# Kernel tuning notes

Measured on AMD Instinct MI355X. Metric: run time of the kernel, lower is better.

The kernel has to match this reference:

```python
import jax, jax.numpy as jnp
import numpy as np

B, N, D, NH, L, DFF = 2, 2048, 256, 8, 4, 1024
DH = D // NH
FACTOR = 0.5 / float(np.sqrt(DH))  # == 1/sqrt(4*DH), matches q/k feature dim 4*d_head
EPS = 1e-5


def _ln(x, g, b):
    m = x.mean(-1, keepdims=True)
    v = ((x - m) ** 2).mean(-1, keepdims=True)
    return (x - m) * jax.lax.rsqrt(v + EPS) * g + b


def setup_inputs() -> dict:
    key = jax.random.key(0)
    ks = jax.random.split(key, 16)
    s = 0.05
    r = lambda i, shape: jax.random.normal(ks[i], shape, dtype=jnp.float32)
    return {
        "H": r(0, (B, N, D)),
        "V": r(1, (B, N, 3, D)),
        "D_batch": r(2, (B, N, N)),
        "rbf_feat": r(3, (L, B, 1, N, N)),
        "H_mask": jnp.ones((B, N), dtype=bool),
        "ln1_g": jnp.ones((L, D)), "ln1_b": jnp.zeros((L, D)),
        "ln2_g": jnp.ones((L, D)), "ln2_b": jnp.zeros((L, D)),
        "Wq": r(4, (L, D, 4 * D)) * s, "bq": jnp.zeros((L, 4 * D)),
        "Wk": r(5, (L, D, 4 * D)) * s, "bk": jnp.zeros((L, 4 * D)),
        "Wv": r(6, (L, D, D)) * s, "bv": jnp.zeros((L, D)),
        "Wvv": r(7, (L, D, D)) * s,
        "Wo": r(8, (L, D, D)) * s, "bo": jnp.zeros((L, D)),
        "Wvo": r(9, (L, D, D)) * s,
        "Wlv": r(10, (L, D, 2 * D)) * s,
        "W1": r(11, (L, 2 * D, DFF)) * s, "b1": jnp.zeros((L, DFF)),
        "W2": r(12, (L, DFF, 2 * D)) * s, "b2": jnp.zeros((L, 2 * D)),
    }


def _stack_forward(H, V, D_batch, rbf_feat, H_mask, ln1_g, ln1_b, ln2_g, ln2_b,
                   Wq, bq, Wk, bk, Wv, bv, Wvv, Wo, bo, Wvo, Wlv, W1, b1, W2, b2):
    b, n = H.shape[:2]
    mask = H_mask[:, None, None, :]       # [B,1,1,N] masks key columns
    base_bias = D_batch[:, None]          # [B,1,N,N]

    def step(carry, xs):
        H, V = carry
        (rbf, g1, be1, g2, be2, wq, bq_, wk, bk_, wv, bv_, wvv,
         wo, bo_, wvo, wlv, w1, b1_, w2, b2_) = xs
        # --- self-attention sublayer (pre-LN on scalar stream only) ---
        Hn = _ln(H, g1, be1)
        Hq = (Hn @ wq + bq_).reshape(b, n, NH, 4 * DH)
        Hk = (Hn @ wk + bk_).reshape(b, n, NH, 4 * DH)
        Hv = (Hn @ wv + bv_).reshape(b, n, NH, DH)
        Vv = (V @ wvv).reshape(b, n, 3, NH, DH)
        Vv = jnp.swapaxes(Vv, 2, 3).reshape(b, n, NH, 3 * DH)
        V_attn = jnp.concatenate([Hv, Vv], axis=-1)        # [B,N,H,4*DH]
        bias = jnp.where(mask, rbf + base_bias, -jnp.inf)  # [B,1,N,N]
        scores = jnp.einsum('bnhd,bmhd->bhnm', Hq, Hk) * FACTOR + bias
        attn = jax.nn.softmax(scores, axis=-1)
        res = jnp.einsum('bhnm,bmhd->bnhd', attn, V_attn)  # [B,N,H,4*DH]
        H_res = res[..., :DH].reshape(b, n, D)
        V_res = jnp.swapaxes(res[..., DH:].reshape(b, n, NH, 3, DH), 2, 3).reshape(b, n, 3, D)
        H = H + (H_res @ wo + bo_)
        V = V + V_res @ wvo
        # --- GVP FFN sublayer (pre-LN on scalar stream only) ---
        Hn = _ln(H, g2, be2)
        Vp = V @ wlv                                       # [B,N,3,2D]
        V1, V2 = Vp[..., :D], Vp[..., D:]
        scaler = jnp.concatenate([Hn, jnp.linalg.norm(V1, axis=-2)], axis=-1)
        sc = jax.nn.silu(scaler @ w1 + b1_) @ w2 + b2_
        H = H + sc[..., :D]
        V = V + sc[..., D:][..., None, :] * V2             # vector_act='none'
        return (H, V), None

    xs = (rbf_feat, ln1_g, ln1_b, ln2_g, ln2_b, Wq, bq, Wk, bk, Wv, bv, Wvv,
          Wo, bo, Wvo, Wlv, W1, b1, W2, b2)
    (H, V), _ = jax.lax.scan(step, (H, V), xs)
    return H, V


def reference(H, V, D_batch, rbf_feat, H_mask, ln1_g, ln1_b, ln2_g, ln2_b,
              Wq, bq, Wk, bk, Wv, bv, Wvv, Wo, bo, Wvo, Wlv, W1, b1, W2, b2):
    return _stack_forward(H, V, D_batch, rbf_feat, H_mask, ln1_g, ln1_b, ln2_g, ln2_b,
                          Wq, bq, Wk, bk, Wv, bv, Wvv, Wo, bo, Wvo, Wlv, W1, b1, W2, b2)
```

## Files before the change

kernel.cpp:

```cpp
#include <hip/hip_runtime.h>
#include <math.h>

static constexpr int B_  = 2;
static constexpr int N_  = 2048;
static constexpr int D_  = 256;
static constexpr int NH_ = 8;
static constexpr int L_  = 4;
static constexpr int DH_ = 32;
static constexpr int DQ_ = 128;
static constexpr float FACTOR_ = 0.08838834764831845f;
static constexpr float LOG2E_  = 1.4426950408889634f;
static constexpr float EPS_ = 1e-5f;

typedef short    short8   __attribute__((ext_vector_type(8)));
typedef unsigned short us4 __attribute__((ext_vector_type(4)));
typedef unsigned short us8 __attribute__((ext_vector_type(8)));
typedef float    f32x4    __attribute__((ext_vector_type(4)));
typedef unsigned short us;

__device__ __forceinline__ us f2b(float f) {
  unsigned u = __float_as_uint(f);
  unsigned r = u + 0x7FFF + ((u >> 16) & 1);
  return (us)(r >> 16);
}
__device__ __forceinline__ float b2f(us u) {
  return __uint_as_float(((unsigned)u) << 16);
}
__device__ __forceinline__ float e2(float x) {
  return __builtin_amdgcn_exp2f(x);
}
__device__ __forceinline__ void gl_lds16(const void* g, void* l) {
  __builtin_amdgcn_global_load_lds(
      (const __attribute__((address_space(1))) void*)g,
      (__attribute__((address_space(3))) void*)l, 16, 0, 0);
}

__global__ __launch_bounds__(256) void ln_kernel(const float* __restrict__ X,
    const float* __restrict__ g, const float* __restrict__ b,
    us* __restrict__ Y) {
  __shared__ float r1[256], r2[256];
  int row = blockIdx.x, tid = threadIdx.x;
  float x = X[(size_t)row * D_ + tid];
  r1[tid] = x; r2[tid] = x * x;
  __syncthreads();
  for (int s = 128; s > 0; s >>= 1) {
    if (tid < s) { r1[tid] += r1[tid + s]; r2[tid] += r2[tid + s]; }
    __syncthreads();
  }
  float mean = r1[0] * (1.0f / D_);
  float var  = r2[0] * (1.0f / D_) - mean * mean;
  float inv  = rsqrtf(var + EPS_);
  Y[(size_t)row * D_ + tid] = f2b((x - mean) * inv * g[tid] + b[tid]);
}

__global__ __launch_bounds__(256) void conv_bf16(const float* __restrict__ X,
    us* __restrict__ Y) {
  size_t i = ((size_t)blockIdx.x * 256 + threadIdx.x) * 4;
  float4 v = *(const float4*)&X[i];
  us4 o = { f2b(v.x), f2b(v.y), f2b(v.z), f2b(v.w) };
  *(us4*)&Y[i] = o;
}

__global__ __launch_bounds__(256) void biascomb(const float* __restrict__ R,
    const float* __restrict__ Dq, us* __restrict__ Out) {
  size_t i = ((size_t)blockIdx.x * 256 + threadIdx.x) * 8;
  float4 r0 = *(const float4*)&R[i];
  float4 r1 = *(const float4*)&R[i + 4];
  float4 d0 = *(const float4*)&Dq[i];
  float4 d1 = *(const float4*)&Dq[i + 4];
  us8 o = { f2b((r0.x + d0.x) * LOG2E_), f2b((r0.y + d0.y) * LOG2E_),
            f2b((r0.z + d0.z) * LOG2E_), f2b((r0.w + d0.w) * LOG2E_),
            f2b((r1.x + d1.x) * LOG2E_), f2b((r1.y + d1.y) * LOG2E_),
            f2b((r1.z + d1.z) * LOG2E_), f2b((r1.w + d1.w) * LOG2E_) };
  *(us8*)&Out[i] = o;
}

struct WConvDesc {
  const float* src[9];
  unsigned dst[9];
  int K[9];
  int N[9];
  int start[10];
};
__global__ __launch_bounds__(256) void wconv_kernel(WConvDesc d, us* __restrict__ Wb) {
  __shared__ float T[64][65];
  int bid = blockIdx.x, tid = threadIdx.x;
  int j = 0;
  #pragma unroll
  for (int q = 0; q < 8; q++) if (bid >= d.start[q + 1]) j = q + 1;
  int t = bid - d.start[j];
  int K = d.K[j], N = d.N[j];
  int tpr = N >> 6;
  int tk = t / tpr, tn = t - tk * tpr;
  const float* src = d.src[j];
  us* dst = Wb + d.dst[j];
  #pragma unroll
  for (int i = 0; i < 4; i++) {
    int r = i * 16 + (tid >> 4), c = (tid & 15) * 4;
    *(float4*)&T[r][c] = *(const float4*)&src[(size_t)(tk * 64 + r) * N + tn * 64 + c];
  }
  __syncthreads();
  #pragma unroll
  for (int i = 0; i < 4; i++) {
    int n = i * 16 + (tid >> 4), k = (tid & 15) * 4;
    us4 o = { f2b(T[k][n]), f2b(T[k + 1][n]), f2b(T[k + 2][n]), f2b(T[k + 3][n]) };
    *(us4*)&dst[(size_t)(tn * 64 + n) * K + tk * 64 + k] = o;
  }
}

template<int BIG, int BIAS, int ACC, int SILU, int WF, int WB, int QKV>
__global__ __launch_bounds__(256, 2) void gemm_v2(const us* __restrict__ A,
    const us* __restrict__ Wt, const float* __restrict__ bias,
    const float* __restrict__ bias2, const float* __restrict__ bias3,
    float* __restrict__ Cf, us* __restrict__ Cb,
    int M, int K, int Nc, float oscale) {
  constexpr int BM  = BIG ? 128 : 64;
  constexpr int NF  = BIG ? 4 : 2;
  constexpr int WS  = NF * 16;
  constexpr int NLD = BM / 32;
  __shared__ us As[2][BM * 64];
  __shared__ us Bs[2][BM * 64];
  const int tid = threadIdx.x;
  const int w = tid >> 6, l = tid & 63;
  const int lx = l & 15, ly = l >> 4;
  const int wr = w >> 1, wc = w & 1;
  const int bn = blockIdx.x, bm = blockIdx.y;
  const int swz = (lx & 7) << 4;
  const char* Ag = (const char*)A + (size_t)(bm * BM) * K * 2;
  const char* Bg = (const char*)Wt + (size_t)(bn * BM) * K * 2;
  const size_t rowb = (size_t)K * 2;

  #define GSTAGE(buf, k0)                                                     \
    do {                                                                      \
      _Pragma("unroll")                                                       \
      for (int j = 0; j < NLD; j++) {                                         \
        int o = j * 4096 + tid * 16;                                          \
        int r = o >> 7, cb = o & 127;                                         \
        int sc = cb ^ ((r & 7) << 4);                                         \
        gl_lds16(Ag + (size_t)r * rowb + (size_t)(k0) * 2 + sc,               \
                 &As[buf][(j * 4096 + w * 1024) >> 1]);                       \
        gl_lds16(Bg + (size_t)r * rowb + (size_t)(k0) * 2 + sc,               \
                 &Bs[buf][(j * 4096 + w * 1024) >> 1]);                       \
      }                                                                       \
    } while (0)

  f32x4 acc[NF][NF];
  #pragma unroll
  for (int i = 0; i < NF; i++)
    #pragma unroll
    for (int j = 0; j < NF; j++) acc[i][j] = (f32x4){0.f, 0.f, 0.f, 0.f};

  int cur = 0;
  GSTAGE(0, 0);
  __syncthreads();
  for (int k0 = 0; k0 < K; k0 += 64) {
    if (k0 + 64 < K) GSTAGE(cur ^ 1, k0 + 64);
    #pragma unroll
    for (int s = 0; s < 2; s++) {
      short8 af[NF], bf[NF];
      #pragma unroll
      for (int mt = 0; mt < NF; mt++)
        af[mt] = *(const short8*)
            &As[cur][(((wr * WS + mt * 16 + lx) * 128) + ((s * 64 + ly * 16) ^ swz)) >> 1];
      #pragma unroll
      for (int nt = 0; nt < NF; nt++)
        bf[nt] = *(const short8*)
            &Bs[cur][(((wc * WS + nt * 16 + lx) * 128) + ((s * 64 + ly * 16) ^ swz)) >> 1];
      __builtin_amdgcn_s_setprio(1);
      #pragma unroll
      for (int mt = 0; mt < NF; mt++)
        #pragma unroll
        for (int nt = 0; nt < NF; nt++)
          acc[mt][nt] = __builtin_amdgcn_mfma_f32_16x16x32_bf16(af[mt], bf[nt], acc[mt][nt], 0, 0, 0);
      __builtin_amdgcn_s_setprio(0);
    }
    __syncthreads();
    cur ^= 1;
  }
  #undef GSTAGE

  #pragma unroll
  for (int nt = 0; nt < NF; nt++) {
    const int n = bn * BM + wc * WS + nt * 16 + lx;
    float bval = 0.f, osc = oscale;
    if (QKV) {
      if (n < 1024)      { bval = bias[n]; }
      else if (n < 2048) { bval = bias2[n - 1024]; osc = 1.0f; }
      else               { bval = bias3[n - 2048]; osc = 1.0f; }
    } else if (BIAS) {
      bval = bias[n];
    }
    #pragma unroll
    for (int mt = 0; mt < NF; mt++) {
      #pragma unroll
      for (int r = 0; r < 4; r++) {
        const int m = bm * BM + wr * WS + mt * 16 + ly * 4 + r;
        float v = acc[mt][nt][r] + bval;
        if (SILU) v = v / (1.f + __expf(-v));
        size_t idx = (size_t)m * Nc + n;
        if (ACC) v += Cf[idx];
        if (WF) Cf[idx] = v;
        if (WB) Cb[idx] = f2b(v * osc);
      }
    }
  }
}

__global__ __launch_bounds__(256, 2) void gemm_wo(const us* __restrict__ Hres,
    const us* __restrict__ Vres, const us* __restrict__ WtO,
    const us* __restrict__ WtVO, const float* __restrict__ bo,
    float* __restrict__ Hs, float* __restrict__ Vs, us* __restrict__ Vb) {
  constexpr int K = 256, Nc = 256;
  __shared__ us As[2][64 * 64];
  __shared__ us Bs[2][64 * 64];
  const int tid = threadIdx.x;
  const int w = tid >> 6, l = tid & 63;
  const int lx = l & 15, ly = l >> 4;
  const int wr = w >> 1, wc = w & 1;
  const int bn = blockIdx.x, bm = blockIdx.y;
  const bool isH = bm < 64;
  const int mb = isH ? bm : bm - 64;
  const int swz = (lx & 7) << 4;
  const char* Ag = (const char*)(isH ? Hres : Vres) + (size_t)(mb * 64) * K * 2;
  const char* Bg = (const char*)(isH ? WtO : WtVO) + (size_t)(bn * 64) * K * 2;
  const size_t rowb = (size_t)K * 2;

  #define GSTAGE(buf, k0)                                                     \
    do {                                                                      \
      _Pragma("unroll")                                                       \
      for (int j = 0; j < 2; j++) {                                           \
        int o = j * 4096 + tid * 16;                                          \
        int r = o >> 7, cb = o & 127;                                         \
        int sc = cb ^ ((r & 7) << 4);                                         \
        gl_lds16(Ag + (size_t)r * rowb + (size_t)(k0) * 2 + sc,               \
                 &As[buf][(j * 4096 + w * 1024) >> 1]);                       \
        gl_lds16(Bg + (size_t)r * rowb + (size_t)(k0) * 2 + sc,               \
                 &Bs[buf][(j * 4096 + w * 1024) >> 1]);                       \
      }                                                                       \
    } while (0)

  f32x4 acc[2][2];
  #pragma unroll
  for (int i = 0; i < 2; i++)
    #pragma unroll
    for (int j = 0; j < 2; j++) acc[i][j] = (f32x4){0.f, 0.f, 0.f, 0.f};

  int cur = 0;
  GSTAGE(0, 0);
  __syncthreads();
  for (int k0 = 0; k0 < K; k0 += 64) {
    if (k0 + 64 < K) GSTAGE(cur ^ 1, k0 + 64);
    #pragma unroll
    for (int s = 0; s < 2; s++) {
      short8 af[2], bf[2];
      #pragma unroll
      for (int mt = 0; mt < 2; mt++)
        af[mt] = *(const short8*)
            &As[cur][(((wr * 32 + mt * 16 + lx) * 128) + ((s * 64 + ly * 16) ^ swz)) >> 1];
      #pragma unroll
      for (int nt = 0; nt < 2; nt++)
        bf[nt] = *(const short8*)
            &Bs[cur][(((wc * 32 + nt * 16 + lx) * 128) + ((s * 64 + ly * 16) ^ swz)) >> 1];
      __builtin_amdgcn_s_setprio(1);
      #pragma unroll
      for (int mt = 0; mt < 2; mt++)
        #pragma unroll
        for (int nt = 0; nt < 2; nt++)
          acc[mt][nt] = __builtin_amdgcn_mfma_f32_16x16x32_bf16(af[mt], bf[nt], acc[mt][nt], 0, 0, 0);
      __builtin_amdgcn_s_setprio(0);
    }
    __syncthreads();
    cur ^= 1;
  }
  #undef GSTAGE

  #pragma unroll
  for (int nt = 0; nt < 2; nt++) {
    const int n = bn * 64 + wc * 32 + nt * 16 + lx;
    const float bval = isH ? bo[n] : 0.f;
    #pragma unroll
    for (int mt = 0; mt < 2; mt++) {
      #pragma unroll
      for (int r = 0; r < 4; r++) {
        const int m = mb * 64 + wr * 32 + mt * 16 + ly * 4 + r;
        size_t idx = (size_t)m * Nc + n;
        float v = acc[mt][nt][r] + bval;
        if (isH) {
          Hs[idx] += v;
        } else {
          float nv = Vs[idx] + v;
          Vs[idx] = nv;
          Vb[idx] = f2b(nv);
        }
      }
    }
  }
}

__global__ __launch_bounds__(256, 2) void gemm_w2(const us* __restrict__ A,
    const us* __restrict__ Wt, const float* __restrict__ b2,
    const float* __restrict__ Vp, float* __restrict__ Hs,
    float* __restrict__ Vs, us* __restrict__ Vb) {
  constexpr int K = 1024, Nc = 512;
  __shared__ us As[2][64 * 64];
  __shared__ us Bs[2][64 * 64];
  const int tid = threadIdx.x;
  const int w = tid >> 6, l = tid & 63;
  const int lx = l & 15, ly = l >> 4;
  const int wr = w >> 1, wc = w & 1;
  const int bn = blockIdx.x, bm = blockIdx.y;
  const int swz = (lx & 7) << 4;
  const char* Ag = (const char*)A + (size_t)(bm * 64) * K * 2;
  const char* Bg = (const char*)Wt + (size_t)(bn * 64) * K * 2;
  const size_t rowb = (size_t)K * 2;

  #define GSTAGE(buf, k0)                                                     \
    do {                                                                      \
      _Pragma("unroll")                                                       \
      for (int j = 0; j < 2; j++) {                                           \
        int o = j * 4096 + tid * 16;                                          \
        int r = o >> 7, cb = o & 127;                                         \
        int sc = cb ^ ((r & 7) << 4);                                         \
        gl_lds16(Ag + (size_t)r * rowb + (size_t)(k0) * 2 + sc,               \
                 &As[buf][(j * 4096 + w * 1024) >> 1]);                       \
        gl_lds16(Bg + (size_t)r * rowb + (size_t)(k0) * 2 + sc,               \
                 &Bs[buf][(j * 4096 + w * 1024) >> 1]);                       \
      }                                                                      \
    } while (0)

  f32x4 acc[2][2];
  #pragma unroll
  for (int i = 0; i < 2; i++)
    #pragma unroll
    for (int j = 0; j < 2; j++) acc[i][j] = (f32x4){0.f, 0.f, 0.f, 0.f};

  int cur = 0;
  GSTAGE(0, 0);
  __syncthreads();
  for (int k0 = 0; k0 < K; k0 += 64) {
    if (k0 + 64 < K) GSTAGE(cur ^ 1, k0 + 64);
    #pragma unroll
    for (int s = 0; s < 2; s++) {
      short8 af[2], bf[2];
      #pragma unroll
      for (int mt = 0; mt < 2; mt++)
        af[mt] = *(const short8*)
            &As[cur][(((wr * 32 + mt * 16 + lx) * 128) + ((s * 64 + ly * 16) ^ swz)) >> 1];
      #pragma unroll
      for (int nt = 0; nt < 2; nt++)
        bf[nt] = *(const short8*)
            &Bs[cur][(((wc * 32 + nt * 16 + lx) * 128) + ((s * 64 + ly * 16) ^ swz)) >> 1];
      __builtin_amdgcn_s_setprio(1);
      #pragma unroll
      for (int mt = 0; mt < 2; mt++)
        #pragma unroll
        for (int nt = 0; nt < 2; nt++)
          acc[mt][nt] = __builtin_amdgcn_mfma_f32_16x16x32_bf16(af[mt], bf[nt], acc[mt][nt], 0, 0, 0);
      __builtin_amdgcn_s_setprio(0);
    }
    __syncthreads();
    cur ^= 1;
  }
  #undef GSTAGE

  const bool isH = (bn < 4);
  #pragma unroll
  for (int nt = 0; nt < 2; nt++) {
    const int n = bn * 64 + wc * 32 + nt * 16 + lx;
    const float bval = b2[n];
    #pragma unroll
    for (int mt = 0; mt < 2; mt++) {
      #pragma unroll
      for (int r = 0; r < 4; r++) {
        const int m = bm * 64 + wr * 32 + mt * 16 + ly * 4 + r;
        float v = acc[mt][nt][r] + bval;
        if (isH) {
          Hs[(size_t)m * D_ + n] += v;
        } else {
          const int j = n - 256;
          #pragma unroll
          for (int c = 0; c < 3; c++) {
            size_t vi = ((size_t)m * 3 + c) * D_ + j;
            float nv = Vs[vi] + v * Vp[((size_t)m * 3 + c) * 512 + 256 + j];
            Vs[vi] = nv;
            Vb[vi] = f2b(nv);
          }
        }
      }
    }
  }
}

__global__ __launch_bounds__(256) void pack_vattn_t(const us* __restrict__ QKVb,
    const us* __restrict__ Vv, us* __restrict__ Vt) {
  __shared__ us T[64][136];
  const int bid = blockIdx.x;
  const int nt = bid & 31, hh = (bid >> 5) & 7, b = bid >> 8;
  const int n0 = nt * 64;
  const int tid = threadIdx.x;
  {
    const int nn = tid >> 2, part = tid & 3;
    const size_t row = (size_t)(b * N_ + n0 + nn);
    const us* src = (part == 0) ? (QKVb + row * 2304 + 2048 + hh * DH_)
                                : (Vv + (row * 3 + (part - 1)) * D_ + hh * DH_);
    #pragma unroll
    for (int jj = 0; jj < 32; jj += 8)
      *(us8*)&T[nn][part * 32 + jj] = *(const us8*)(src + jj);
  }
  __syncthreads();
  const int d = tid >> 1, half = tid & 1;
  size_t ob = ((size_t)(b * NH_ + hh) * DQ_ + d) * (size_t)N_ + n0 + half * 32;
  #pragma unroll
  for (int i = 0; i < 32; i += 8) {
    us8 o;
    #pragma unroll
    for (int e = 0; e < 8; e++) o[e] = T[half * 32 + i + e][d];
    *(us8*)&Vt[ob + i] = o;
  }
}

__global__ __launch_bounds__(256, 2) void attn_mfma(
    const us* __restrict__ QKVb,
    const us* __restrict__ Vtb,
    const us* __restrict__ bias,
    us* __restrict__ Hres,
    us* __restrict__ Vres) {
  __shared__ us Kt[2][8192];
  __shared__ us Vt[2][8192];
  __shared__ us Plds[4][16][72];
  const int bid = blockIdx.x;
  const int h  = bid >> 6;
  const int g  = bid & 63;
  const int b  = g >> 5;
  const int qt = g & 31;
  const int tid = threadIdx.x;
  const int w  = tid >> 6;
  const int l  = tid & 63;
  const int lx = l & 15;
  const int ly = l >> 4;
  const int qrow = qt * 64 + w * 16 + lx;
  const int swz = (lx & 7) << 4;

  short8 qf[4];
  {
    const us* qp = QKVb + (size_t)(b * N_ + qrow) * 2304 + h * DQ_ + ly * 8;
    #pragma unroll
    for (int s = 0; s < 4; s++) qf[s] = *(const short8*)(qp + s * 32);
  }
  const char* kg = (const char*)QKVb + (size_t)b * N_ * 4608 + 2048 + h * 256;
  const char* vg = (const char*)(Vtb + ((size_t)(b * NH_ + h) * DQ_) * (size_t)N_);
  const us* bbase = bias + ((size_t)b * N_ + qrow) * N_;

  #define STAGE(buf, m0)                                                      \
    do {                                                                      \
      _Pragma("unroll")                                                       \
      for (int j = 0; j < 4; j++) {                                           \
        int o = j * 4096 + tid * 16;                                          \
        int r = o >> 8, cb = o & 255;                                         \
        int scb = cb ^ ((r & 7) << 4);                                        \
        gl_lds16(kg + (size_t)((m0) + r) * 4608 + scb,                        \
                 &Kt[buf][(j * 4096 + w * 1024) >> 1]);                       \
      }                                                                       \
      _Pragma("unroll")                                                       \
      for (int j = 0; j < 4; j++) {                                           \
        int o = j * 4096 + tid * 16;                                          \
        int r = o >> 7, cb = o & 127;                                         \
        int scb = cb ^ ((r & 7) << 4);                                        \
        gl_lds16(vg + (size_t)r * (N_ * 2) + (size_t)(m0) * 2 + scb,          \
                 &Vt[buf][(j * 4096 + w * 1024) >> 1]);                       \
      }                                                                       \
    } while (0)

  float m_run = -3.0e38f, l_run = 0.f;
  f32x4 oacc[8];
  #pragma unroll
  for (int i = 0; i < 8; i++) oacc[i] = (f32x4){0.f, 0.f, 0.f, 0.f};

  int cur = 0;
  STAGE(0, 0);
  us4 bb[4];
  #pragma unroll
  for (int t = 0; t < 4; t++) bb[t] = *(const us4*)(bbase + t * 16 + ly * 4);
  __syncthreads();

  for (int mc0 = 0; mc0 < N_; mc0 += 64) {
    us4 bbn[4];
    if (mc0 + 64 < N_) {
      STAGE(cur ^ 1, mc0 + 64);
      #pragma unroll
      for (int t = 0; t < 4; t++)
        bbn[t] = *(const us4*)(bbase + mc0 + 64 + t * 16 + ly * 4);
    }
    f32x4 sacc[4];
    #pragma unroll
    for (int t = 0; t < 4; t++) sacc[t] = (f32x4){0.f, 0.f, 0.f, 0.f};
    __builtin_amdgcn_s_setprio(1);
    #pragma unroll
    for (int t = 0; t < 4; t++) {
      #pragma unroll
      for (int s = 0; s < 4; s++) {
        const short8 kf = *(const short8*)
            &Kt[cur][((t * 16 + lx) * 256 + ((s * 64 + ly * 16) ^ swz)) >> 1];
        sacc[t] = __builtin_amdgcn_mfma_f32_16x16x32_bf16(kf, qf[s], sacc[t], 0, 0, 0);
      }
    }
    __builtin_amdgcn_s_setprio(0);
    float pvv[16];
    #pragma unroll
    for (int t = 0; t < 4; t++) {
      pvv[t*4+0] = sacc[t][0] + b2f(bb[t][0]);
      pvv[t*4+1] = sacc[t][1] + b2f(bb[t][1]);
      pvv[t*4+2] = sacc[t][2] + b2f(bb[t][2]);
      pvv[t*4+3] = sacc[t][3] + b2f(bb[t][3]);
    }
    float a8[8], a4[4];
    #pragma unroll
    for (int i = 0; i < 8; i++) a8[i] = fmaxf(pvv[i], pvv[i + 8]);
    #pragma unroll
    for (int i = 0; i < 4; i++) a4[i] = fmaxf(a8[i], a8[i + 4]);
    float mloc = fmaxf(fmaxf(a4[0], a4[1]), fmaxf(a4[2], a4[3]));
    if (!__all(mloc - m_run <= 11.54f)) {
      mloc = fmaxf(mloc, __shfl_xor(mloc, 16, 64));
      mloc = fmaxf(mloc, __shfl_xor(mloc, 32, 64));
      float m_new = fmaxf(m_run, mloc);
      float scale = e2(m_run - m_new);
      l_run *= scale;
      #pragma unroll
      for (int i = 0; i < 8; i++) {
        oacc[i][0] *= scale; oacc[i][1] *= scale;
        oacc[i][2] *= scale; oacc[i][3] *= scale;
      }
      m_run = m_new;
    }
    float s8[8], s4[4];
    #pragma unroll
    for (int i = 0; i < 16; i++) pvv[i] = e2(pvv[i] - m_run);
    #pragma unroll
    for (int i = 0; i < 8; i++) s8[i] = pvv[i] + pvv[i + 8];
    #pragma unroll
    for (int i = 0; i < 4; i++) s4[i] = s8[i] + s8[i + 4];
    l_run += (s4[0] + s4[1]) + (s4[2] + s4[3]);
    #pragma unroll
    for (int t = 0; t < 4; t++) {
      us4 pk = { f2b(pvv[t*4+0]), f2b(pvv[t*4+1]), f2b(pvv[t*4+2]), f2b(pvv[t*4+3]) };
      *(us4*)&Plds[w][lx][t * 16 + ly * 4] = pk;
    }
    short8 pf0 = *(const short8*)&Plds[w][lx][ly * 8];
    short8 pf1 = *(const short8*)&Plds[w][lx][32 + ly * 8];
    __builtin_amdgcn_s_setprio(1);
    #pragma unroll
    for (int dt = 0; dt < 8; dt++) {
      const int rb = (dt * 16 + lx) * 128;
      const short8 vf0 = *(const short8*)&Vt[cur][(rb + ((ly * 16) ^ swz)) >> 1];
      const short8 vf1 = *(const short8*)&Vt[cur][(rb + ((64 + ly * 16) ^ swz)) >> 1];
      oacc[dt] = __builtin_amdgcn_mfma_f32_16x16x32_bf16(vf0, pf0, oacc[dt], 0, 0, 0);
      oacc[dt] = __builtin_amdgcn_mfma_f32_16x16x32_bf16(vf1, pf1, oacc[dt], 0, 0, 0);
    }
    __builtin_amdgcn_s_setprio(0);
    __syncthreads();
    cur ^= 1;
    if (mc0 + 64 < N_) {
      #pragma unroll
      for (int t = 0; t < 4; t++) bb[t] = bbn[t];
    }
  }
  #undef STAGE
  l_run += __shfl_xor(l_run, 16, 64);
  l_run += __shfl_xor(l_run, 32, 64);
  float inv = 1.0f / l_run;
  const size_t row = (size_t)(b * N_ + qrow);
  #pragma unroll
  for (int dt = 0; dt < 8; dt++) {
    const int d0 = dt * 16 + ly * 4;
    us4 pk = { f2b(oacc[dt][0] * inv), f2b(oacc[dt][1] * inv),
               f2b(oacc[dt][2] * inv), f2b(oacc[dt][3] * inv) };
    if (d0 < 32) {
      *(us4*)&Hres[row * D_ + h * DH_ + d0] = pk;
    } else {
      const int c = (d0 - DH_) >> 5, dd = (d0 - DH_) & 31;
      *(us4*)&Vres[(row * 3 + c) * D_ + h * DH_ + dd] = pk;
    }
  }
}

__global__ __launch_bounds__(256) void ln2scaler(const float* __restrict__ H,
    const float* __restrict__ g, const float* __restrict__ b,
    const float* __restrict__ Vp, us* __restrict__ scal) {
  __shared__ float r1[256], r2[256];
  size_t row = blockIdx.x;
  int j = threadIdx.x;
  float x = H[row * D_ + j];
  r1[j] = x; r2[j] = x * x;
  __syncthreads();
  for (int s = 128; s > 0; s >>= 1) {
    if (j < s) { r1[j] += r1[j + s]; r2[j] += r2[j + s]; }
    __syncthreads();
  }
  float mean = r1[0] * (1.0f / D_);
  float var  = r2[0] * (1.0f / D_) - mean * mean;
  float inv  = rsqrtf(var + EPS_);
  scal[row * 512 + j] = f2b((x - mean) * inv * g[j] + b[j]);
  float a  = Vp[(row * 3 + 0) * 512 + j];
  float c1 = Vp[(row * 3 + 1) * 512 + j];
  float c2 = Vp[(row * 3 + 2) * 512 + j];
  scal[row * 512 + D_ + j] = f2b(sqrtf(a * a + c1 * c1 + c2 * c2));
}

extern "C" void kernel_launch(void* const* d_in, const int* in_sizes, int n_in,
                              void* d_out, int out_size, void* d_ws, size_t ws_size,
                              hipStream_t stream) {
  const float* H_in = (const float*)d_in[0];
  const float* V_in = (const float*)d_in[1];
  const float* Db   = (const float*)d_in[2];
  const float* rbf  = (const float*)d_in[3];
  const float* ln1g = (const float*)d_in[5];
  const float* ln1b = (const float*)d_in[6];
  const float* ln2g = (const float*)d_in[7];
  const float* ln2b = (const float*)d_in[8];
  const float* Wq  = (const float*)d_in[9];
  const float* bq  = (const float*)d_in[10];
  const float* Wk  = (const float*)d_in[11];
  const float* bk  = (const float*)d_in[12];
  const float* Wv  = (const float*)d_in[13];
  const float* bv  = (const float*)d_in[14];
  const float* Wvv = (const float*)d_in[15];
  const float* Wo  = (const float*)d_in[16];
  const float* bo  = (const float*)d_in[17];
  const float* Wvo = (const float*)d_in[18];
  const float* Wlv = (const float*)d_in[19];
  const float* W1  = (const float*)d_in[20];
  const float* b1  = (const float*)d_in[21];
  const float* W2  = (const float*)d_in[22];
  const float* b2  = (const float*)d_in[23];

  const size_t HN = (size_t)B_ * N_ * D_;
  const size_t VN = HN * 3;
  float* Hs = (float*)d_out;
  float* Vs = (float*)d_out + HN;
  float* ws = (float*)d_ws;
  us*    bias_b = (us*)ws;
  us*    Wb     = (us*)(ws + 4194304);
  us*    Vb     = (us*)(ws + 5177344);
  us*    Hnb    = (us*)(ws + 6750208);
  us*    QKVb   = (us*)(ws + 7274496);
  us*    Vtb    = (us*)(ws + 11993088);
  us*    Vvb    = (us*)(ws + 14090240);
  us*    Hres_b = (us*)(ws + 6750208);
  us*    Vres_b = (us*)(ws + 14090240);
  float* Vp     = ws + 7274496;
  us*    scal_b = (us*)(ws + 13565952);
  us*    midb   = (us*)(ws + 15014528);

  hipMemcpyAsync(Hs, H_in, HN * sizeof(float), hipMemcpyDeviceToDevice, stream);
  hipMemcpyAsync(Vs, V_in, VN * sizeof(float), hipMemcpyDeviceToDevice, stream);
  conv_bf16<<<3072, 256, 0, stream>>>(V_in, Vb);

  const int ROWS  = B_ * N_;
  static const int wKs[9] = {256,256,256,256,256,256,256,512,1024};
  static const int wNs[9] = {1024,1024,256,256,256,256,512,1024,512};
  static const unsigned wOff[9] = {0,262144,524288,589824,655360,720896,786432,917504,1441792};
  static const int wStart[10] = {0,64,128,144,160,176,192,224,352,480};

  for (int l = 0; l < L_; ++l) {
    WConvDesc dsc;
    const float* srcs[9] = {
      Wq  + (size_t)l * 256 * 1024, Wk  + (size_t)l * 256 * 1024,
      Wv  + (size_t)l * 256 * 256,  Wvv + (size_t)l * 256 * 256,
      Wo  + (size_t)l * 256 * 256,  Wvo + (size_t)l * 256 * 256,
      Wlv + (size_t)l * 256 * 512,  W1  + (size_t)l * 512 * 1024,
      W2  + (size_t)l * 1024 * 512 };
    for (int j = 0; j < 9; j++) {
      dsc.src[j] = srcs[j]; dsc.dst[j] = wOff[j];
      dsc.K[j] = wKs[j]; dsc.N[j] = wNs[j]; dsc.start[j] = wStart[j];
    }
    dsc.start[9] = wStart[9];
    wconv_kernel<<<480, 256, 0, stream>>>(dsc, Wb);
    biascomb<<<4096, 256, 0, stream>>>(rbf + (size_t)l * B_ * N_ * N_, Db, bias_b);
    if (l == 0)
      ln_kernel<<<ROWS, 256, 0, stream>>>(Hs, ln1g, ln1b, Hnb);

    gemm_v2<1,0,0,0,0,1,1><<<dim3(18, 32), 256, 0, stream>>>(
        Hnb, Wb + wOff[0], bq + l * 1024, bk + l * 1024, bv + l * 256,
        nullptr, QKVb, 4096, 256, 2304, FACTOR_ * LOG2E_);
    gemm_v2<0,0,0,0,0,1,0><<<dim3(4, 192), 256, 0, stream>>>(
        Vb, Wb + wOff[3], nullptr, nullptr, nullptr, nullptr, Vvb, 12288, 256, 256, 1.f);
    pack_vattn_t<<<512, 256, 0, stream>>>(QKVb, Vvb, Vtb);
    attn_mfma<<<512, 256, 0, stream>>>(QKVb, Vtb, bias_b, Hres_b, Vres_b);
    gemm_wo<<<dim3(4, 256), 256, 0, stream>>>(
        Hres_b, Vres_b, Wb + wOff[4], Wb + wOff[5], bo + l * 256, Hs, Vs, Vb);
    gemm_v2<0,0,0,0,1,0,0><<<dim3(8, 192), 256, 0, stream>>>(
        Vb, Wb + wOff[6], nullptr, nullptr, nullptr, Vp, nullptr, 12288, 256, 512, 1.f);
    ln2scaler<<<ROWS, 256, 0, stream>>>(Hs, ln2g + l * D_, ln2b + l * D_, Vp, scal_b);
    gemm_v2<0,1,0,1,0,1,0><<<dim3(16, 64), 256, 0, stream>>>(
        scal_b, Wb + wOff[7], b1 + l * 1024, nullptr, nullptr, nullptr, midb, 4096, 512, 1024, 1.f);
    gemm_w2<<<dim3(8, 64), 256, 0, stream>>>(
        midb, Wb + wOff[8], b2 + l * 512, Vp, Hs, Vs, Vb);
    if (l < 3)
      ln_kernel<<<ROWS, 256, 0, stream>>>(Hs, ln1g + (l + 1) * D_,
                                          ln1b + (l + 1) * D_, Hnb);
  }
}
```

Baseline: 808.6 us.

## Register-staged single-buffer K/V in attention and rectangular GEMM tiles for W1

Measured after the change: 785.9 us. 1.03x faster.

```diff
diff --git a/kernel.cpp b/kernel.cpp
--- a/kernel.cpp
+++ b/kernel.cpp
@@ -108,18 +108,17 @@
   }
 }
 
-template<int BIG, int BIAS, int ACC, int SILU, int WF, int WB, int QKV>
+template<int BM, int BN, int BIAS, int ACC, int SILU, int WF, int WB, int QKV>
 __global__ __launch_bounds__(256, 2) void gemm_v2(const us* __restrict__ A,
     const us* __restrict__ Wt, const float* __restrict__ bias,
     const float* __restrict__ bias2, const float* __restrict__ bias3,
     float* __restrict__ Cf, us* __restrict__ Cb,
     int M, int K, int Nc, float oscale) {
-  constexpr int BM  = BIG ? 128 : 64;
-  constexpr int NF  = BIG ? 4 : 2;
-  constexpr int WS  = NF * 16;
-  constexpr int NLD = BM / 32;
+  constexpr int NFM = BM / 32, NFN = BN / 32;
+  constexpr int WSM = NFM * 16, WSN = NFN * 16;
+  constexpr int NLA = BM / 32, NLB = BN / 32;
   __shared__ us As[2][BM * 64];
-  __shared__ us Bs[2][BM * 64];
+  __shared__ us Bs[2][BN * 64];
   const int tid = threadIdx.x;
   const int w = tid >> 6, l = tid & 63;
   const int lx = l & 15, ly = l >> 4;
@@ -127,28 +126,34 @@
   const int bn = blockIdx.x, bm = blockIdx.y;
   const int swz = (lx & 7) << 4;
   const char* Ag = (const char*)A + (size_t)(bm * BM) * K * 2;
-  const char* Bg = (const char*)Wt + (size_t)(bn * BM) * K * 2;
+  const char* Bg = (const char*)Wt + (size_t)(bn * BN) * K * 2;
   const size_t rowb = (size_t)K * 2;
 
   #define GSTAGE(buf, k0)                                                     \
     do {                                                                      \
       _Pragma("unroll")                                                       \
-      for (int j = 0; j < NLD; j++) {                                         \
+      for (int j = 0; j < NLA; j++) {                                         \
         int o = j * 4096 + tid * 16;                                          \
         int r = o >> 7, cb = o & 127;                                         \
         int sc = cb ^ ((r & 7) << 4);                                         \
         gl_lds16(Ag + (size_t)r * rowb + (size_t)(k0) * 2 + sc,               \
                  &As[buf][(j * 4096 + w * 1024) >> 1]);                       \
+      }                                                                       \
+      _Pragma("unroll")                                                       \
+      for (int j = 0; j < NLB; j++) {                                         \
+        int o = j * 4096 + tid * 16;                                          \
+        int r = o >> 7, cb = o & 127;                                         \
+        int sc = cb ^ ((r & 7) << 4);                                         \
         gl_lds16(Bg + (size_t)r * rowb + (size_t)(k0) * 2 + sc,               \
                  &Bs[buf][(j * 4096 + w * 1024) >> 1]);                       \
       }                                                                       \
     } while (0)
 
-  f32x4 acc[NF][NF];
-  #pragma unroll
-  for (int i = 0; i < NF; i++)
-    #pragma unroll
-    for (int j = 0; j < NF; j++) acc[i][j] = (f32x4){0.f, 0.f, 0.f, 0.f};
+  f32x4 acc[NFM][NFN];
+  #pragma unroll
+  for (int i = 0; i < NFM; i++)
+    #pragma unroll
+    for (int j = 0; j < NFN; j++) acc[i][j] = (f32x4){0.f, 0.f, 0.f, 0.f};
 
   int cur = 0;
   GSTAGE(0, 0);
@@ -157,20 +162,20 @@
     if (k0 + 64 < K) GSTAGE(cur ^ 1, k0 + 64);
     #pragma unroll
     for (int s = 0; s < 2; s++) {
-      short8 af[NF], bf[NF];
-      #pragma unroll
-      for (int mt = 0; mt < NF; mt++)
+      short8 af[NFM], bf[NFN];
+      #pragma unroll
+      for (int mt = 0; mt < NFM; mt++)
         af[mt] = *(const short8*)
-            &As[cur][(((wr * WS + mt * 16 + lx) * 128) + ((s * 64 + ly * 16) ^ swz)) >> 1];
-      #pragma unroll
-      for (int nt = 0; nt < NF; nt++)
+            &As[cur][(((wr * WSM + mt * 16 + lx) * 128) + ((s * 64 + ly * 16) ^ swz)) >> 1];
+      #pragma unroll
+      for (int nt = 0; nt < NFN; nt++)
         bf[nt] = *(const short8*)
-            &Bs[cur][(((wc * WS + nt * 16 + lx) * 128) + ((s * 64 + ly * 16) ^ swz)) >> 1];
+            &Bs[cur][(((wc * WSN + nt * 16 + lx) * 128) + ((s * 64 + ly * 16) ^ swz)) >> 1];
       __builtin_amdgcn_s_setprio(1);
       #pragma unroll
-      for (int mt = 0; mt < NF; mt++)
+      for (int mt = 0; mt < NFM; mt++)
         #pragma unroll
-        for (int nt = 0; nt < NF; nt++)
+        for (int nt = 0; nt < NFN; nt++)
           acc[mt][nt] = __builtin_amdgcn_mfma_f32_16x16x32_bf16(af[mt], bf[nt], acc[mt][nt], 0, 0, 0);
       __builtin_amdgcn_s_setprio(0);
     }
@@ -180,8 +185,8 @@
   #undef GSTAGE
 
   #pragma unroll
-  for (int nt = 0; nt < NF; nt++) {
-    const int n = bn * BM + wc * WS + nt * 16 + lx;
+  for (int nt = 0; nt < NFN; nt++) {
+    const int n = bn * BN + wc * WSN + nt * 16 + lx;
     float bval = 0.f, osc = oscale;
     if (QKV) {
       if (n < 1024)      { bval = bias[n]; }
@@ -191,10 +196,10 @@
       bval = bias[n];
     }
     #pragma unroll
-    for (int mt = 0; mt < NF; mt++) {
+    for (int mt = 0; mt < NFM; mt++) {
       #pragma unroll
       for (int r = 0; r < 4; r++) {
-        const int m = bm * BM + wr * WS + mt * 16 + ly * 4 + r;
+        const int m = bm * BM + wr * WSM + mt * 16 + ly * 4 + r;
         float v = acc[mt][nt][r] + bval;
         if (SILU) v = v / (1.f + __expf(-v));
         size_t idx = (size_t)m * Nc + n;
@@ -301,7 +306,7 @@
     const us* __restrict__ Wt, const float* __restrict__ b2,
     const float* __restrict__ Vp, float* __restrict__ Hs,
     float* __restrict__ Vs, us* __restrict__ Vb) {
-  constexpr int K = 1024, Nc = 512;
+  constexpr int K = 1024;
   __shared__ us As[2][64 * 64];
   __shared__ us Bs[2][64 * 64];
   const int tid = threadIdx.x;
@@ -419,14 +424,14 @@
   }
 }
 
-__global__ __launch_bounds__(256, 2) void attn_mfma(
+__global__ __launch_bounds__(256, 3) void attn_mfma(
     const us* __restrict__ QKVb,
     const us* __restrict__ Vtb,
     const us* __restrict__ bias,
     us* __restrict__ Hres,
     us* __restrict__ Vres) {
-  __shared__ us Kt[2][8192];
-  __shared__ us Vt[2][8192];
+  __shared__ us Kt[8192];
+  __shared__ us Vt[8192];
   __shared__ us Plds[4][16][72];
   const int bid = blockIdx.x;
   const int h  = bid >> 6;
@@ -451,23 +456,26 @@
   const char* vg = (const char*)(Vtb + ((size_t)(b * NH_ + h) * DQ_) * (size_t)N_);
   const us* bbase = bias + ((size_t)b * N_ + qrow) * N_;
 
-  #define STAGE(buf, m0)                                                      \
+  us8 kreg[4], vreg[4];
+  #define LOADKV(m0)                                                          \
     do {                                                                      \
       _Pragma("unroll")                                                       \
       for (int j = 0; j < 4; j++) {                                           \
         int o = j * 4096 + tid * 16;                                          \
-        int r = o >> 8, cb = o & 255;                                         \
-        int scb = cb ^ ((r & 7) << 4);                                        \
-        gl_lds16(kg + (size_t)((m0) + r) * 4608 + scb,                        \
-                 &Kt[buf][(j * 4096 + w * 1024) >> 1]);                       \
+        int rk = o >> 8, ck = o & 255;                                        \
+        kreg[j] = *(const us8*)(kg + (size_t)((m0) + rk) * 4608 +             \
+                                (ck ^ ((rk & 7) << 4)));                      \
+        int rv = o >> 7, cv = o & 127;                                        \
+        vreg[j] = *(const us8*)(vg + (size_t)rv * (N_ * 2) +                  \
+                                (size_t)(m0) * 2 + (cv ^ ((rv & 7) << 4)));   \
       }                                                                       \
+    } while (0)
+  #define WRITEKV()                                                           \
+    do {                                                                      \
       _Pragma("unroll")                                                       \
       for (int j = 0; j < 4; j++) {                                           \
-        int o = j * 4096 + tid * 16;                                          \
-        int r = o >> 7, cb = o & 127;                                         \
-        int scb = cb ^ ((r & 7) << 4);                                        \
-        gl_lds16(vg + (size_t)r * (N_ * 2) + (size_t)(m0) * 2 + scb,          \
-                 &Vt[buf][(j * 4096 + w * 1024) >> 1]);                       \
+        *(us8*)&Kt[j * 2048 + tid * 8] = kreg[j];                             \
+        *(us8*)&Vt[j * 2048 + tid * 8] = vreg[j];                             \
       }                                                                       \
     } while (0)
 
@@ -476,8 +484,9 @@
   #pragma unroll
   for (int i = 0; i < 8; i++) oacc[i] = (f32x4){0.f, 0.f, 0.f, 0.f};
 
-  int cur = 0;
-  STAGE(0, 0);
+  LOADKV(0);
+  WRITEKV();
+  LOADKV(64);
   us4 bb[4];
   #pragma unroll
   for (int t = 0; t < 4; t++) bb[t] = *(const us4*)(bbase + t * 16 + ly * 4);
@@ -486,7 +495,6 @@
   for (int mc0 = 0; mc0 < N_; mc0 += 64) {
     us4 bbn[4];
     if (mc0 + 64 < N_) {
-      STAGE(cur ^ 1, mc0 + 64);
       #pragma unroll
       for (int t = 0; t < 4; t++)
         bbn[t] = *(const us4*)(bbase + mc0 + 64 + t * 16 + ly * 4);
@@ -500,7 +508,7 @@
       #pragma unroll
       for (int s = 0; s < 4; s++) {
         const short8 kf = *(const short8*)
-            &Kt[cur][((t * 16 + lx) * 256 + ((s * 64 + ly * 16) ^ swz)) >> 1];
+            &Kt[((t * 16 + lx) * 256 + ((s * 64 + ly * 16) ^ swz)) >> 1];
         sacc[t] = __builtin_amdgcn_mfma_f32_16x16x32_bf16(kf, qf[s], sacc[t], 0, 0, 0);
       }
     }
@@ -551,20 +559,23 @@
     #pragma unroll
     for (int dt = 0; dt < 8; dt++) {
       const int rb = (dt * 16 + lx) * 128;
-      const short8 vf0 = *(const short8*)&Vt[cur][(rb + ((ly * 16) ^ swz)) >> 1];
-      const short8 vf1 = *(const short8*)&Vt[cur][(rb + ((64 + ly * 16) ^ swz)) >> 1];
+      const short8 vf0 = *(const short8*)&Vt[(rb + ((ly * 16) ^ swz)) >> 1];
+      const short8 vf1 = *(const short8*)&Vt[(rb + ((64 + ly * 16) ^ swz)) >> 1];
       oacc[dt] = __builtin_amdgcn_mfma_f32_16x16x32_bf16(vf0, pf0, oacc[dt], 0, 0, 0);
       oacc[dt] = __builtin_amdgcn_mfma_f32_16x16x32_bf16(vf1, pf1, oacc[dt], 0, 0, 0);
     }
     __builtin_amdgcn_s_setprio(0);
     __syncthreads();
-    cur ^= 1;
     if (mc0 + 64 < N_) {
+      WRITEKV();
+      if (mc0 + 128 < N_) LOADKV(mc0 + 128);
       #pragma unroll
       for (int t = 0; t < 4; t++) bb[t] = bbn[t];
-    }
-  }
-  #undef STAGE
+      __syncthreads();
+    }
+  }
+  #undef LOADKV
+  #undef WRITEKV
   l_run += __shfl_xor(l_run, 16, 64);
   l_run += __shfl_xor(l_run, 32, 64);
   float inv = 1.0f / l_run;
@@ -679,19 +690,19 @@
     if (l == 0)
       ln_kernel<<<ROWS, 256, 0, stream>>>(Hs, ln1g, ln1b, Hnb);
 
-    gemm_v2<1,0,0,0,0,1,1><<<dim3(18, 32), 256, 0, stream>>>(
+    gemm_v2<128,128,0,0,0,0,1,1><<<dim3(18, 32), 256, 0, stream>>>(
         Hnb, Wb + wOff[0], bq + l * 1024, bk + l * 1024, bv + l * 256,
         nullptr, QKVb, 4096, 256, 2304, FACTOR_ * LOG2E_);
-    gemm_v2<0,0,0,0,0,1,0><<<dim3(4, 192), 256, 0, stream>>>(
+    gemm_v2<64,64,0,0,0,0,1,0><<<dim3(4, 192), 256, 0, stream>>>(
         Vb, Wb + wOff[3], nullptr, nullptr, nullptr, nullptr, Vvb, 12288, 256, 256, 1.f);
     pack_vattn_t<<<512, 256, 0, stream>>>(QKVb, Vvb, Vtb);
     attn_mfma<<<512, 256, 0, stream>>>(QKVb, Vtb, bias_b, Hres_b, Vres_b);
     gemm_wo<<<dim3(4, 256), 256, 0, stream>>>(
         Hres_b, Vres_b, Wb + wOff[4], Wb + wOff[5], bo + l * 256, Hs, Vs, Vb);
-    gemm_v2<0,0,0,0,1,0,0><<<dim3(8, 192), 256, 0, stream>>>(
+    gemm_v2<64,64,0,0,0,1,0,0><<<dim3(8, 192), 256, 0, stream>>>(
         Vb, Wb + wOff[6], nullptr, nullptr, nullptr, Vp, nullptr, 12288, 256, 512, 1.f);
     ln2scaler<<<ROWS, 256, 0, stream>>>(Hs, ln2g + l * D_, ln2b + l * D_, Vp, scal_b);
-    gemm_v2<0,1,0,1,0,1,0><<<dim3(16, 64), 256, 0, stream>>>(
+    gemm_v2<128,64,1,0,1,0,1,0><<<dim3(16, 32), 256, 0, stream>>>(
         scal_b, Wb + wOff[7], b1 + l * 1024, nullptr, nullptr, nullptr, midb, 4096, 512, 1024, 1.f);
     gemm_w2<<<dim3(8, 64), 256, 0, stream>>>(
         midb, Wb + wOff[8], b2 + l * 512, Vp, Hs, Vs, Vb);
```
